# Kernel tuning notes

Measured on AMD Instinct MI355X. Metric: run time of the kernel, lower is better.

## Reference

```python
import jax, jax.numpy as jnp
import numpy as np

HEADS = 16
HEAD_DIM = 64
DIM = 1024
WH, WW = 32, 32
ROPE_DIM = 32  # = HEAD_DIM // 2
ROPE_BASE = 10000
EPS = 1e-6


def _rope_cache():
    # theta: [ROPE_DIM//2]
    theta = 1.0 / (ROPE_BASE ** (jnp.arange(0, ROPE_DIM, 2, dtype=jnp.float32)[: ROPE_DIM // 2] / ROPE_DIM))
    n = WH * WW
    idx = jnp.arange(n, dtype=jnp.float32)
    x_pos = idx % WW
    y_pos = idx // WW
    freqs = jnp.concatenate([x_pos[:, None] * theta[None, :], y_pos[:, None] * theta[None, :]], axis=-1)  # [n, ROPE_DIM]
    return jnp.cos(freqs), jnp.sin(freqs)


def _apply_rope(x, cos, sin):
    # x: [b, h, n, HEAD_DIM] -> pairs [b, h, n, ROPE_DIM, 2]
    xf = x.astype(jnp.float32).reshape(*x.shape[:-1], -1, 2)
    x0, x1 = xf[..., 0], xf[..., 1]
    c = cos[None, None, :, :]
    s = sin[None, None, :, :]
    out = jnp.stack([x0 * c - x1 * s, x1 * c + x0 * s], axis=-1)
    return out.reshape(*x.shape).astype(x.dtype)


def setup_inputs() -> dict:
    key = jax.random.key(0)
    ks = jax.random.split(key, 5)
    b, n = 16, WH * WW
    inner = HEADS * HEAD_DIM
    return {
        "x": jax.random.normal(ks[0], (b, n, DIM), dtype=jnp.float32),
        "t": jax.random.normal(ks[1], (b, DIM), dtype=jnp.float32),
        "norm_w": jnp.ones((DIM,), dtype=jnp.float32),
        "mod_w": jax.random.normal(ks[2], (2 * DIM, DIM), dtype=jnp.float32) * (DIM ** -0.5),
        "qkv_w": jax.random.normal(ks[3], (3 * inner, DIM), dtype=jnp.float32) * (DIM ** -0.5),
        "wo_w": jax.random.normal(ks[4], (DIM, inner), dtype=jnp.float32) * (inner ** -0.5),
    }


def reference(x, t, norm_w, mod_w, qkv_w, wo_w):
    b, n, dim = x.shape
    scale = HEAD_DIM ** -0.5

    # Modulated RMSNorm
    xf = x.astype(jnp.float32)
    xn = (xf * jax.lax.rsqrt(jnp.mean(xf * xf, axis=-1, keepdims=True) + EPS)).astype(x.dtype) * norm_w
    mod = t @ mod_w.T  # [b, 2*dim]
    sc, sh = mod[:, :dim], mod[:, dim:]
    h = xn * (1.0 + sc[:, None, :]) + sh[:, None, :]

    # QKV projection; rearrange 'b n (h d) -> b h n d' with d = 3*HEAD_DIM, THEN chunk
    qkv = h @ qkv_w.T  # [b, n, 3*inner]
    qkv = qkv.reshape(b, n, HEADS, 3 * HEAD_DIM).transpose(0, 2, 1, 3)  # [b, H, n, 3*hd]
    q, k, v = qkv[..., :HEAD_DIM], qkv[..., HEAD_DIM:2 * HEAD_DIM], qkv[..., 2 * HEAD_DIM:]

    # 2D axial RoPE on q, k
    cos, sin = _rope_cache()
    q = _apply_rope(q, cos, sin)
    k = _apply_rope(k, cos, sin)

    # SDPA (non-causal)
    attn = jax.nn.softmax(jnp.einsum('bhqd,bhkd->bhqk', q * scale, k), axis=-1)
    out = jnp.einsum('bhqk,bhkd->bhqd', attn, v)  # [b, H, n, hd]
    out = out.transpose(0, 2, 1, 3).reshape(b, n, HEADS * HEAD_DIM)
    return out @ wo_w.T
```

## Files before the change

kernel.cpp:

```cpp
#include <hip/hip_runtime.h>
#include <stdint.h>

typedef __bf16    bf16x8 __attribute__((ext_vector_type(8)));
typedef float     f32x4  __attribute__((ext_vector_type(4)));
typedef _Float16  f16;
typedef _Float16  f16x2  __attribute__((ext_vector_type(2)));
typedef _Float16  f16x4  __attribute__((ext_vector_type(4)));
typedef _Float16  f16x8  __attribute__((ext_vector_type(8)));

#define DEV __device__ __forceinline__

DEV ushort f2bf(float f) {
  union { float f; uint32_t u; } v; v.f = f;
  uint32_t u = v.u;
  return (ushort)((u + 0x7fffu + ((u >> 16) & 1u)) >> 16);
}

DEV f16x2 cvt_pkrtz(float a, float b) {
  return __builtin_bit_cast(f16x2, __builtin_amdgcn_cvt_pkrtz(a, b));
}

DEV void async16(const void* g, void* l) {
  __builtin_amdgcn_global_load_lds(
      (__attribute__((address_space(1))) void*)(uintptr_t)g,
      (__attribute__((address_space(3))) void*)(uint32_t)(uintptr_t)l,
      16, 0, 0);
}

__global__ __launch_bounds__(256)
void prep_kernel(const float* __restrict__ t, const float* __restrict__ mw,
                 float* __restrict__ mod,
                 const float* __restrict__ qkvw, ushort* __restrict__ wqk,
                 ushort* __restrict__ wv,
                 const float* __restrict__ wow, ushort* __restrict__ wowb) {
  const int id = blockIdx.x;
  const int tid = threadIdx.x;
  if (id < 2048) {
    const int j = id;
    const int w = tid >> 6, lane = tid & 63;
    float wr[16];
#pragma unroll
    for (int i = 0; i < 16; ++i) wr[i] = mw[(size_t)j * 1024 + lane + i * 64];
#pragma unroll
    for (int bb = 0; bb < 4; ++bb) {
      int b = w * 4 + bb;
      float s = 0.f;
#pragma unroll
      for (int i = 0; i < 16; ++i) s += wr[i] * t[b * 1024 + lane + i * 64];
#pragma unroll
      for (int m = 32; m >= 1; m >>= 1) s += __shfl_xor(s, m, 64);
      if (lane == 0) mod[b * 2048 + j] = s;
    }
  } else if (id < 5120) {
    const int j = id - 2048;
    uint32_t hd = (uint32_t)j / 192u;
    uint32_t rem = (uint32_t)j - hd * 192u;
    ushort* dst = (rem < 128u) ? (wqk + (size_t)(hd * 128u + rem) * 1024)
                               : (wv + (size_t)(hd * 64u + (rem - 128u)) * 1024);
    float4 v = ((const float4*)(qkvw + (size_t)j * 1024))[tid];
    ushort4 o;
    o.x = f2bf(v.x); o.y = f2bf(v.y); o.z = f2bf(v.z); o.w = f2bf(v.w);
    ((ushort4*)dst)[tid] = o;
  } else {
    const int i = (id - 5120) * 256 + tid;
    float4 v = ((const float4*)wow)[i];
    ushort4 o;
    o.x = f2bf(v.x); o.y = f2bf(v.y); o.z = f2bf(v.z); o.w = f2bf(v.w);
    ((ushort4*)wowb)[i] = o;
  }
}

__global__ __launch_bounds__(256)
void rms_mod_kernel(const float* __restrict__ x, const float* __restrict__ nw,
                    const float* __restrict__ mod, ushort* __restrict__ h) {
  int row = blockIdx.x;
  int b = row >> 10;
  int tid = threadIdx.x;
  const float4 xv = *(const float4*)(x + (size_t)row * 1024 + tid * 4);
  float ss = xv.x * xv.x + xv.y * xv.y + xv.z * xv.z + xv.w * xv.w;
#pragma unroll
  for (int m = 32; m >= 1; m >>= 1) ss += __shfl_xor(ss, m, 64);
  __shared__ float red[4];
  int w = tid >> 6, lane = tid & 63;
  if (lane == 0) red[w] = ss;
  __syncthreads();
  float tot = red[0] + red[1] + red[2] + red[3];
  float rn = rsqrtf(tot * (1.f / 1024.f) + 1e-6f);
  float4 wv = *(const float4*)(nw + tid * 4);
  float4 sc = *(const float4*)(mod + (size_t)b * 2048 + tid * 4);
  float4 sh = *(const float4*)(mod + (size_t)b * 2048 + 1024 + tid * 4);
  ushort4 o;
  o.x = f2bf(xv.x * rn * wv.x * (1.f + sc.x) + sh.x);
  o.y = f2bf(xv.y * rn * wv.y * (1.f + sc.y) + sh.y);
  o.z = f2bf(xv.z * rn * wv.z * (1.f + sc.z) + sh.z);
  o.w = f2bf(xv.w * rn * wv.w * (1.f + sc.w) + sh.w);
  *(ushort4*)(h + (size_t)row * 1024 + tid * 4) = o;
}

__global__ __launch_bounds__(512, 2)
void gemm_qkv_kernel(const ushort* __restrict__ hbuf, const ushort* __restrict__ wqk,
                     const ushort* __restrict__ wvw,
                     f16* __restrict__ qb, f16* __restrict__ kb,
                     f16* __restrict__ vtb) {
  __shared__ ushort smem[65536];
  const int id0 = blockIdx.x;
  const int id = (id0 & 7) * 96 + (id0 >> 3);
  int mode, m0, n0;
  const ushort *A, *B;
  if (id < 512) {
    mode = 1; m0 = (id >> 3) * 256; n0 = (id & 7) * 256; A = hbuf; B = wqk;
  } else {
    const int i2 = id - 512;
    mode = 2; n0 = (i2 >> 2) * 256; m0 = (i2 & 3) * 256; A = wvw; B = hbuf;
  }
  const int tid = threadIdx.x;
  const int w = tid >> 6, lane = tid & 63, quad = lane >> 4, l15 = lane & 15;
  const int wm = w >> 2, wn = w & 3;

  const int srow = tid >> 3;
  const int sch  = (tid & 7) ^ (srow & 7);
  const int soff = srow * 1024 + sch * 8;
  const ushort* const Abase = A + (size_t)m0 * 1024;
  const ushort* const Bbase = B + (size_t)n0 * 1024;
  ushort* const As0 = smem;
  ushort* const Bs0 = smem + 32768;
  const int sdst = tid * 8;

#define STG_A(d, t, h) do { \
    async16(Abase + (h) * 131072 + soff + (t) * 64,          As0 + (d) * 16384 + (h) * 8192 + sdst); \
    async16(Abase + (h) * 131072 + 65536 + soff + (t) * 64,  As0 + (d) * 16384 + (h) * 8192 + 4096 + sdst); } while (0)
#define STG_B(d, t, h) do { \
    async16(Bbase + (h) * 131072 + soff + (t) * 64,          Bs0 + (d) * 16384 + (h) * 8192 + sdst); \
    async16(Bbase + (h) * 131072 + 65536 + soff + (t) * 64,  Bs0 + (d) * 16384 + (h) * 8192 + 4096 + sdst); } while (0)

  int aoff[2], boff[2];
#pragma unroll
  for (int kk = 0; kk < 2; ++kk) {
    const int swz = (((kk * 4 + quad) ^ (l15 & 7)) * 8);
    aoff[kk] = (wm * 128 + l15) * 64 + swz;
    boff[kk] = (wn * 64 + l15) * 64 + swz;
  }

  const f32x4 fzero = {0.f, 0.f, 0.f, 0.f};
  f32x4 acc[8][4];
#pragma unroll
  for (int a = 0; a < 8; ++a)
#pragma unroll
    for (int b = 0; b < 4; ++b) acc[a][b] = fzero;

  STG_A(0, 0, 0); STG_A(0, 0, 1); STG_B(0, 0, 0); STG_B(0, 0, 1);
  asm volatile("s_waitcnt vmcnt(0)" ::: "memory");
  __builtin_amdgcn_s_barrier();

  bf16x8 af[4][2];
  bf16x8 bfv[2][2];
#pragma unroll 2
  for (int t = 0; t < 16; ++t) {
    const int cur = t & 1, nxt = cur ^ 1;
    const int tn = (t < 15) ? t + 1 : 15;
    const ushort* Asc = As0 + cur * 16384;
    const ushort* Bsc = Bs0 + cur * 16384;

#pragma unroll
    for (int mf = 0; mf < 4; ++mf)
#pragma unroll
      for (int kk = 0; kk < 2; ++kk)
        af[mf][kk] = *(const bf16x8*)(Asc + mf * 1024 + aoff[kk]);
#pragma unroll
    for (int nf = 0; nf < 2; ++nf)
#pragma unroll
      for (int kk = 0; kk < 2; ++kk)
        bfv[nf][kk] = *(const bf16x8*)(Bsc + nf * 1024 + boff[kk]);
    STG_A(nxt, tn, 0);
    __builtin_amdgcn_s_barrier();
    __builtin_amdgcn_s_setprio(1);
#pragma unroll
    for (int mf = 0; mf < 4; ++mf)
#pragma unroll
      for (int nf = 0; nf < 2; ++nf)
#pragma unroll
        for (int kk = 0; kk < 2; ++kk)
          acc[mf][nf] = __builtin_amdgcn_mfma_f32_16x16x32_bf16(
              af[mf][kk], bfv[nf][kk], acc[mf][nf], 0, 0, 0);
    __builtin_amdgcn_s_setprio(0);
    __builtin_amdgcn_s_barrier();

#pragma unroll
    for (int mf = 0; mf < 4; ++mf)
#pragma unroll
      for (int kk = 0; kk < 2; ++kk)
        af[mf][kk] = *(const bf16x8*)(Asc + (4 + mf) * 1024 + aoff[kk]);
    STG_A(nxt, tn, 1);
    __builtin_amdgcn_s_barrier();
    __builtin_amdgcn_s_setprio(1);
#pragma unroll
    for (int mf = 0; mf < 4; ++mf)
#pragma unroll
      for (int nf = 0; nf < 2; ++nf)
#pragma unroll
        for (int kk = 0; kk < 2; ++kk)
          acc[4 + mf][nf] = __builtin_amdgcn_mfma_f32_16x16x32_bf16(
              af[mf][kk], bfv[nf][kk], acc[4 + mf][nf], 0, 0, 0);
    __builtin_amdgcn_s_setprio(0);
    __builtin_amdgcn_s_barrier();

#pragma unroll
    for (int nf = 0; nf < 2; ++nf)
#pragma unroll
      for (int kk = 0; kk < 2; ++kk)
        bfv[nf][kk] = *(const bf16x8*)(Bsc + (2 + nf) * 1024 + boff[kk]);
    STG_B(nxt, tn, 0);
    __builtin_amdgcn_s_barrier();
    __builtin_amdgcn_s_setprio(1);
#pragma unroll
    for (int mf = 0; mf < 4; ++mf)
#pragma unroll
      for (int nf = 0; nf < 2; ++nf)
#pragma unroll
        for (int kk = 0; kk < 2; ++kk)
          acc[4 + mf][2 + nf] = __builtin_amdgcn_mfma_f32_16x16x32_bf16(
              af[mf][kk], bfv[nf][kk], acc[4 + mf][2 + nf], 0, 0, 0);
    __builtin_amdgcn_s_setprio(0);
    __builtin_amdgcn_s_barrier();

#pragma unroll
    for (int mf = 0; mf < 4; ++mf)
#pragma unroll
      for (int kk = 0; kk < 2; ++kk)
        af[mf][kk] = *(const bf16x8*)(Asc + mf * 1024 + aoff[kk]);
    STG_B(nxt, tn, 1);
    __builtin_amdgcn_s_barrier();
    __builtin_amdgcn_s_setprio(1);
#pragma unroll
    for (int mf = 0; mf < 4; ++mf)
#pragma unroll
      for (int nf = 0; nf < 2; ++nf)
#pragma unroll
        for (int kk = 0; kk < 2; ++kk)
          acc[mf][2 + nf] = __builtin_amdgcn_mfma_f32_16x16x32_bf16(
              af[mf][kk], bfv[nf][kk], acc[mf][2 + nf], 0, 0, 0);
    __builtin_amdgcn_s_setprio(0);
    asm volatile("s_waitcnt vmcnt(0)" ::: "memory");
    __builtin_amdgcn_s_barrier();
  }
#undef STG_A
#undef STG_B

  ushort* eps = smem + w * 8192;
#pragma unroll
  for (int mf = 0; mf < 8; ++mf)
#pragma unroll
    for (int nf = 0; nf < 4; ++nf)
#pragma unroll
      for (int r = 0; r < 4; ++r) {
        const int row_loc = mf * 16 + quad * 4 + r;
        const int col = nf * 16 + l15;
        const int ch = (col >> 3) ^ (row_loc & 7);
        union { f16 h; ushort u; } cv;
        cv.h = (f16)acc[mf][nf][r];
        eps[row_loc * 64 + ch * 8 + (col & 7)] = cv.u;
      }

  const int ch = lane & 7;
  const int rbase = lane >> 3;
  const int gcol = n0 + wn * 64;
  if (mode == 1) {
    const int hd = gcol >> 7, part = (gcol >> 6) & 1;
    const float QS = part ? 1.f : 0.125f * 1.44269504f;
    f16* const outp = part ? kb : qb;
    float th[4];
#pragma unroll
    for (int t2 = 0; t2 < 4; ++t2)
      th[t2] = __expf(-(float)((ch * 4 + t2) & 15) * 0.5756462732485114f);
#pragma unroll
    for (int i = 0; i < 16; ++i) {
      const int row_loc = i * 8 + rbase;
      union { uint4 u4; f16 h[8]; } uv;
      uv.u4 = *(const uint4*)(eps + row_loc * 64 + ((ch ^ (row_loc & 7)) * 8));
      const int m = m0 + wm * 128 + row_loc;
      const int n = m & 1023;
      const float xpos = (float)(n & 31), ypos = (float)(n >> 5);
#pragma unroll
      for (int t2 = 0; t2 < 4; ++t2) {
        const int p = ch * 4 + t2;
        const float pos = (p < 16) ? xpos : ypos;
        float sn, cs;
        __sincosf(pos * th[t2], &sn, &cs);
        const float x0 = (float)uv.h[2 * t2], x1 = (float)uv.h[2 * t2 + 1];
        f16x2 ro = cvt_pkrtz((x0 * cs - x1 * sn) * QS, (x1 * cs + x0 * sn) * QS);
        uv.h[2 * t2] = ro[0];
        uv.h[2 * t2 + 1] = ro[1];
      }
      f16* dst = outp + (((size_t)((m >> 10) * 16 + hd) * 1024 + n) * 64 + ch * 8);
      *(uint4*)dst = uv.u4;
    }
  } else {
    const int b = gcol >> 10, tb = gcol & 1023;
#pragma unroll
    for (int i = 0; i < 16; ++i) {
      const int row_loc = i * 8 + rbase;
      const uint4 v = *(const uint4*)(eps + row_loc * 64 + ((ch ^ (row_loc & 7)) * 8));
      const int m = m0 + wm * 128 + row_loc;
      f16* dst = vtb + ((size_t)(b * 1024 + m) * 1024 + tb + ch * 8);
      *(uint4*)dst = v;
    }
  }
}

__global__ __launch_bounds__(256, 3)
void gemm_wo_kernel(const ushort* __restrict__ A, const ushort* __restrict__ B,
                    float* __restrict__ outf) {
  __shared__ ushort smem[8192];
  ushort* As = smem;
  ushort* Bs = smem + 4096;
  const int K = 1024;
  const int m0 = blockIdx.y * 128, n0 = blockIdx.x * 128;
  const int tid = threadIdx.x;
  const int w = tid >> 6, lane = tid & 63, quad = lane >> 4, l15 = lane & 15;
  const int wm = (w >> 1) * 64, wn = (w & 1) * 64;
  const f32x4 fzero = {0.f, 0.f, 0.f, 0.f};
  f32x4 acc[4][4];
#pragma unroll
  for (int a = 0; a < 4; ++a)
#pragma unroll
    for (int b = 0; b < 4; ++b) acc[a][b] = fzero;

  const int s0 = tid, s1 = 256 + tid;
  const int r0 = s0 >> 2, c0 = (s0 & 3) ^ ((r0 >> 1) & 3);
  const int r1 = s1 >> 2, c1 = (s1 & 3) ^ ((r1 >> 1) & 3);
  const int b0 = m0 >> 10, nb = m0 & 1023;
  const size_t Abase = (size_t)b0 * 16 * 1024 * 64;
  const ushort* Ag0 = A + Abase + (size_t)(nb + r0) * 64 + c0 * 8;
  const ushort* Ag1 = A + Abase + (size_t)(nb + r1) * 64 + c1 * 8;
  const ushort* Bg0 = B + (size_t)(n0 + r0) * K + c0 * 8;
  const ushort* Bg1 = B + (size_t)(n0 + r1) * K + c1 * 8;

  for (int kt = 0; kt < K; kt += 32) {
    const size_t ka = (size_t)(kt >> 6) * 65536 + (size_t)(kt & 63);
    async16(Ag0 + ka, As + s0 * 8);
    async16(Ag1 + ka, As + s1 * 8);
    async16(Bg0 + kt, Bs + s0 * 8);
    async16(Bg1 + kt, Bs + s1 * 8);
    __syncthreads();
    bf16x8 af[4], bfr[4];
#pragma unroll
    for (int tm = 0; tm < 4; ++tm) {
      int r = wm + tm * 16 + l15;
      int cs = quad ^ ((r >> 1) & 3);
      af[tm] = *(const bf16x8*)(As + (r * 4 + cs) * 8);
    }
#pragma unroll
    for (int tn = 0; tn < 4; ++tn) {
      int r = wn + tn * 16 + l15;
      int cs = quad ^ ((r >> 1) & 3);
      bfr[tn] = *(const bf16x8*)(Bs + (r * 4 + cs) * 8);
    }
#pragma unroll
    for (int tm = 0; tm < 4; ++tm)
#pragma unroll
      for (int tn = 0; tn < 4; ++tn)
        acc[tm][tn] = __builtin_amdgcn_mfma_f32_16x16x32_bf16(af[tm], bfr[tn],
                                                              acc[tm][tn], 0, 0, 0);
    __syncthreads();
  }

#pragma unroll
  for (int tm = 0; tm < 4; ++tm)
#pragma unroll
    for (int tn = 0; tn < 4; ++tn) {
      int col = n0 + wn + tn * 16 + l15;
#pragma unroll
      for (int r = 0; r < 4; ++r) {
        int row = m0 + wm + tm * 16 + quad * 4 + r;
        outf[(size_t)row * 1024 + col] = acc[tm][tn][r];
      }
    }
}

__global__ __launch_bounds__(256, 3)
void attn_kernel(const f16* __restrict__ qbuf, const f16* __restrict__ kbuf,
                 const f16* __restrict__ vtbuf, ushort* __restrict__ aout) {
  __shared__ f16 Ks[128 * 64];
  __shared__ f16 Vs[64 * 128];

  const int id = blockIdx.x;
  const int xcd = id & 7, j = id >> 3;
  const int bh = xcd * 32 + (j >> 3);
  const int q0 = (j & 7) * 128;
  const f16* Qg = qbuf + (size_t)bh * 1024 * 64;
  const f16* Kg = kbuf + (size_t)bh * 1024 * 64;
  const f16* Vg = vtbuf + (size_t)bh * 64 * 1024;
  const int tid = threadIdx.x;
  const int w = tid >> 6, lane = tid & 63, quad = lane >> 4, l15 = lane & 15;
  const f32x4 fzero = {0.f, 0.f, 0.f, 0.f};

  f16x8 qf[2][2];
#pragma unroll
  for (int qs = 0; qs < 2; ++qs)
#pragma unroll
    for (int dc = 0; dc < 2; ++dc)
      qf[qs][dc] = *(const f16x8*)(Qg + (size_t)(q0 + w * 32 + qs * 16 + l15) * 64 +
                                   dc * 32 + quad * 8);

  f32x4 oacc[2][4];
#pragma unroll
  for (int qs = 0; qs < 2; ++qs)
#pragma unroll
    for (int ds = 0; ds < 4; ++ds) oacc[qs][ds] = fzero;
  float mrun[2] = {-1e30f, -1e30f}, lrun[2] = {0.f, 0.f};

  for (int kt = 0; kt < 1024; kt += 128) {
#pragma unroll
    for (int i = 0; i < 4; ++i) {
      int u = i * 256 + tid, r = u >> 3, c = u & 7;
      async16(Kg + (size_t)(kt + r) * 64 + (c ^ (r & 7)) * 8, Ks + u * 8);
    }
#pragma unroll
    for (int i = 0; i < 4; ++i) {
      int u = i * 256 + tid, r = u >> 4, c = u & 15;
      async16(Vg + (size_t)r * 1024 + kt + (c ^ (r & 15)) * 8, Vs + u * 8);
    }
    __syncthreads();

    f32x4 sacc[2][8];
#pragma unroll
    for (int qs = 0; qs < 2; ++qs)
#pragma unroll
      for (int ks = 0; ks < 8; ++ks) sacc[qs][ks] = fzero;
#pragma unroll
    for (int ks = 0; ks < 8; ++ks) {
#pragma unroll
      for (int dc = 0; dc < 2; ++dc) {
        int row = ks * 16 + l15;
        int ch = (dc * 4 + quad) ^ (row & 7);
        f16x8 kf = *(const f16x8*)(Ks + row * 64 + ch * 8);
        sacc[0][ks] = __builtin_amdgcn_mfma_f32_16x16x32_f16(kf, qf[0][dc], sacc[0][ks], 0, 0, 0);
        sacc[1][ks] = __builtin_amdgcn_mfma_f32_16x16x32_f16(kf, qf[1][dc], sacc[1][ks], 0, 0, 0);
      }
    }

    f16x4 pf[2][8];
#pragma unroll
    for (int qs = 0; qs < 2; ++qs) {
      const float* sv = (const float*)&sacc[qs][0];
      float mx = fmaxf(sv[0], sv[1]);
#pragma unroll
      for (int k = 2; k < 32; k += 2)
        mx = fmaxf(fmaxf(mx, sv[k]), sv[k + 1]);
      mx = fmaxf(mx, __shfl_xor(mx, 16, 64));
      mx = fmaxf(mx, __shfl_xor(mx, 32, 64));
      float mnew = fmaxf(mrun[qs], mx);
      float alpha = exp2f(mrun[qs] - mnew);
      mrun[qs] = mnew;
      float rs = 0.f;
#pragma unroll
      for (int ks = 0; ks < 8; ++ks) {
        float p0 = exp2f(sacc[qs][ks][0] - mnew);
        float p1 = exp2f(sacc[qs][ks][1] - mnew);
        float p2 = exp2f(sacc[qs][ks][2] - mnew);
        float p3 = exp2f(sacc[qs][ks][3] - mnew);
        rs += (p0 + p1) + (p2 + p3);
        union { f16x4 v; f16x2 h[2]; } pu;
        pu.h[0] = cvt_pkrtz(p0, p1);
        pu.h[1] = cvt_pkrtz(p2, p3);
        pf[qs][ks] = pu.v;
      }
      rs += __shfl_xor(rs, 16, 64);
      rs += __shfl_xor(rs, 32, 64);
      lrun[qs] = lrun[qs] * alpha + rs;
      float ar[4];
#pragma unroll
      for (int r = 0; r < 4; ++r) ar[r] = __shfl(alpha, quad * 4 + r, 64);
#pragma unroll
      for (int ds = 0; ds < 4; ++ds)
#pragma unroll
        for (int r = 0; r < 4; ++r) oacc[qs][ds][r] *= ar[r];
    }

#pragma unroll
    for (int ks = 0; ks < 8; ++ks) {
#pragma unroll
      for (int ds = 0; ds < 4; ++ds) {
        int row = ds * 16 + l15;
        int c16 = ks * 2 + (quad >> 1);
        f16x4 vf = *(const f16x4*)(Vs + row * 128 + ((c16 ^ (row & 15)) * 8) + (quad & 1) * 4);
        oacc[0][ds] = __builtin_amdgcn_mfma_f32_16x16x16f16(pf[0][ks], vf, oacc[0][ds], 0, 0, 0);
        oacc[1][ds] = __builtin_amdgcn_mfma_f32_16x16x16f16(pf[1][ks], vf, oacc[1][ds], 0, 0, 0);
      }
    }
    __syncthreads();
  }

  ushort* eps = (ushort*)Ks + w * 2048;
#pragma unroll
  for (int qs = 0; qs < 2; ++qs) {
    float linv[4];
#pragma unroll
    for (int r = 0; r < 4; ++r) linv[r] = 1.f / __shfl(lrun[qs], quad * 4 + r, 64);
#pragma unroll
    for (int ds = 0; ds < 4; ++ds)
#pragma unroll
      for (int r = 0; r < 4; ++r) {
        int row_loc = qs * 16 + quad * 4 + r;
        int col = ds * 16 + l15;
        int ch = (col >> 3) ^ (row_loc & 7);
        eps[row_loc * 64 + ch * 8 + (col & 7)] = f2bf(oacc[qs][ds][r] * linv[r]);
      }
  }
  __syncthreads();
  const size_t obase = ((size_t)bh * 1024 + q0 + w * 32) * 64;
#pragma unroll
  for (int i = 0; i < 4; ++i) {
    int row_loc = i * 8 + (lane >> 3);
    int ch = lane & 7;
    uint4 v = *(const uint4*)(eps + row_loc * 64 + ((ch ^ (row_loc & 7)) * 8));
    *(uint4*)(aout + obase + row_loc * 64 + ch * 8) = v;
  }
}

extern "C" void kernel_launch(void* const* d_in, const int* in_sizes, int n_in,
                              void* d_out, int out_size, void* d_ws, size_t ws_size,
                              hipStream_t stream) {
  const float* x    = (const float*)d_in[0];
  const float* t    = (const float*)d_in[1];
  const float* nw   = (const float*)d_in[2];
  const float* mw   = (const float*)d_in[3];
  const float* qkvw = (const float*)d_in[4];
  const float* wow  = (const float*)d_in[5];
  float* out = (float*)d_out;
  char* ws = (char*)d_ws;

  float*  modbuf  = (float*)(ws);
  ushort* hbuf    = (ushort*)(ws + 131072);
  ushort* wqk_b   = (ushort*)(ws + 33685504);
  ushort* wv_b    = (ushort*)(ws + 37879808);
  ushort* wow_b   = (ushort*)(ws + 39976960);
  f16*    qbuf    = (f16*)(ws + 42074112);
  f16*    kbuf    = (f16*)(ws + 75628544);
  f16*    vtbuf   = (f16*)(ws + 109182976);
  ushort* abuf    = (ushort*)(ws + 142737408);

  prep_kernel<<<dim3(6144), dim3(256), 0, stream>>>(
      t, mw, modbuf, qkvw, wqk_b, wv_b, wow, wow_b);
  rms_mod_kernel<<<dim3(16384), dim3(256), 0, stream>>>(x, nw, modbuf, hbuf);
  gemm_qkv_kernel<<<dim3(768), dim3(512), 0, stream>>>(
      hbuf, wqk_b, wv_b, qbuf, kbuf, vtbuf);
  attn_kernel<<<dim3(2048), dim3(256), 0, stream>>>(qbuf, kbuf, vtbuf, abuf);
  gemm_wo_kernel<<<dim3(8, 128), dim3(256), 0, stream>>>(abuf, wow_b, out);
}
```

Before: 437.4 us.

## Double-buffer attention K/V tiles, lazy softmax rescale, fast exp/rcp, V bank swizzle

The attention kernel now double-buffers K and V tiles in shared memory, prefetching the next tile with async loads while the current one is computed. This doubles LDS use, so the occupancy target drops from 3 to 2 blocks. Softmax now skips the running-max rescale unless the max grows by more than 8, and uses hardware exp2 and rcp intrinsics. The V-transpose store swaps 8-byte halves on odd rows, and the PV loads use a matching half index to reduce LDS bank conflicts. The lazy rescale lets unnormalised values grow up to 2^8, which carries some fp16 overflow risk for P accumulation.

```diff
diff --git a/kernel.cpp b/kernel.cpp
--- a/kernel.cpp
+++ b/kernel.cpp
@@ -299,7 +299,8 @@
 #pragma unroll
     for (int i = 0; i < 16; ++i) {
       const int row_loc = i * 8 + rbase;
-      const uint4 v = *(const uint4*)(eps + row_loc * 64 + ((ch ^ (row_loc & 7)) * 8));
+      uint4 v = *(const uint4*)(eps + row_loc * 64 + ((ch ^ (row_loc & 7)) * 8));
+      if (i & 1) { unsigned t0 = v.x, t1 = v.y; v.x = v.z; v.y = v.w; v.z = t0; v.w = t1; }
       const int m = m0 + wm * 128 + row_loc;
       f16* dst = vtb + ((size_t)(b * 1024 + m) * 1024 + tb + ch * 8);
       *(uint4*)dst = v;
@@ -377,11 +378,11 @@
     }
 }
 
-__global__ __launch_bounds__(256, 3)
+__global__ __launch_bounds__(256, 2)
 void attn_kernel(const f16* __restrict__ qbuf, const f16* __restrict__ kbuf,
                  const f16* __restrict__ vtbuf, ushort* __restrict__ aout) {
-  __shared__ f16 Ks[128 * 64];
-  __shared__ f16 Vs[64 * 128];
+  __shared__ f16 Ks[2][128 * 64];
+  __shared__ f16 Vs[2][64 * 128];
 
   const int id = blockIdx.x;
   const int xcd = id & 7, j = id >> 3;
@@ -409,18 +410,36 @@
     for (int ds = 0; ds < 4; ++ds) oacc[qs][ds] = fzero;
   float mrun[2] = {-1e30f, -1e30f}, lrun[2] = {0.f, 0.f};
 
+#pragma unroll
+  for (int i = 0; i < 4; ++i) {
+    int u = i * 256 + tid, r = u >> 3, c = u & 7;
+    async16(Kg + (size_t)r * 64 + (c ^ (r & 7)) * 8, &Ks[0][u * 8]);
+  }
+#pragma unroll
+  for (int i = 0; i < 4; ++i) {
+    int u = i * 256 + tid, r = u >> 4, c = u & 15;
+    async16(Vg + (size_t)r * 1024 + (c ^ (r & 15)) * 8, &Vs[0][u * 8]);
+  }
+  __syncthreads();
+
+#pragma unroll 2
   for (int kt = 0; kt < 1024; kt += 128) {
-#pragma unroll
-    for (int i = 0; i < 4; ++i) {
-      int u = i * 256 + tid, r = u >> 3, c = u & 7;
-      async16(Kg + (size_t)(kt + r) * 64 + (c ^ (r & 7)) * 8, Ks + u * 8);
-    }
-#pragma unroll
-    for (int i = 0; i < 4; ++i) {
-      int u = i * 256 + tid, r = u >> 4, c = u & 15;
-      async16(Vg + (size_t)r * 1024 + kt + (c ^ (r & 15)) * 8, Vs + u * 8);
-    }
-    __syncthreads();
+    const int cur = (kt >> 7) & 1;
+    if (kt + 128 < 1024) {
+      const int nkt = kt + 128;
+#pragma unroll
+      for (int i = 0; i < 4; ++i) {
+        int u = i * 256 + tid, r = u >> 3, c = u & 7;
+        async16(Kg + (size_t)(nkt + r) * 64 + (c ^ (r & 7)) * 8, &Ks[cur ^ 1][u * 8]);
+      }
+#pragma unroll
+      for (int i = 0; i < 4; ++i) {
+        int u = i * 256 + tid, r = u >> 4, c = u & 15;
+        async16(Vg + (size_t)r * 1024 + nkt + (c ^ (r & 15)) * 8, &Vs[cur ^ 1][u * 8]);
+      }
+    }
+    const f16* Ksc = Ks[cur];
+    const f16* Vsc = Vs[cur];
 
     f32x4 sacc[2][8];
 #pragma unroll
@@ -433,7 +452,7 @@
       for (int dc = 0; dc < 2; ++dc) {
         int row = ks * 16 + l15;
         int ch = (dc * 4 + quad) ^ (row & 7);
-        f16x8 kf = *(const f16x8*)(Ks + row * 64 + ch * 8);
+        f16x8 kf = *(const f16x8*)(Ksc + row * 64 + ch * 8);
         sacc[0][ks] = __builtin_amdgcn_mfma_f32_16x16x32_f16(kf, qf[0][dc], sacc[0][ks], 0, 0, 0);
         sacc[1][ks] = __builtin_amdgcn_mfma_f32_16x16x32_f16(kf, qf[1][dc], sacc[1][ks], 0, 0, 0);
       }
@@ -449,16 +468,27 @@
         mx = fmaxf(fmaxf(mx, sv[k]), sv[k + 1]);
       mx = fmaxf(mx, __shfl_xor(mx, 16, 64));
       mx = fmaxf(mx, __shfl_xor(mx, 32, 64));
-      float mnew = fmaxf(mrun[qs], mx);
-      float alpha = exp2f(mrun[qs] - mnew);
-      mrun[qs] = mnew;
+      if (__any(mx - mrun[qs] > 8.f)) {
+        float mnew = fmaxf(mrun[qs], mx);
+        float alpha = __builtin_amdgcn_exp2f(mrun[qs] - mnew);
+        mrun[qs] = mnew;
+        lrun[qs] *= alpha;
+        float ar[4];
+#pragma unroll
+        for (int r = 0; r < 4; ++r) ar[r] = __shfl(alpha, quad * 4 + r, 64);
+#pragma unroll
+        for (int ds = 0; ds < 4; ++ds)
+#pragma unroll
+          for (int r = 0; r < 4; ++r) oacc[qs][ds][r] *= ar[r];
+      }
+      const float mnew = mrun[qs];
       float rs = 0.f;
 #pragma unroll
       for (int ks = 0; ks < 8; ++ks) {
-        float p0 = exp2f(sacc[qs][ks][0] - mnew);
-        float p1 = exp2f(sacc[qs][ks][1] - mnew);
-        float p2 = exp2f(sacc[qs][ks][2] - mnew);
-        float p3 = exp2f(sacc[qs][ks][3] - mnew);
+        float p0 = __builtin_amdgcn_exp2f(sacc[qs][ks][0] - mnew);
+        float p1 = __builtin_amdgcn_exp2f(sacc[qs][ks][1] - mnew);
+        float p2 = __builtin_amdgcn_exp2f(sacc[qs][ks][2] - mnew);
+        float p3 = __builtin_amdgcn_exp2f(sacc[qs][ks][3] - mnew);
         rs += (p0 + p1) + (p2 + p3);
         union { f16x4 v; f16x2 h[2]; } pu;
         pu.h[0] = cvt_pkrtz(p0, p1);
@@ -467,14 +497,7 @@
       }
       rs += __shfl_xor(rs, 16, 64);
       rs += __shfl_xor(rs, 32, 64);
-      lrun[qs] = lrun[qs] * alpha + rs;
-      float ar[4];
-#pragma unroll
-      for (int r = 0; r < 4; ++r) ar[r] = __shfl(alpha, quad * 4 + r, 64);
-#pragma unroll
-      for (int ds = 0; ds < 4; ++ds)
-#pragma unroll
-        for (int r = 0; r < 4; ++r) oacc[qs][ds][r] *= ar[r];
+      lrun[qs] += rs;
     }
 
 #pragma unroll
@@ -483,7 +506,8 @@
       for (int ds = 0; ds < 4; ++ds) {
         int row = ds * 16 + l15;
         int c16 = ks * 2 + (quad >> 1);
-        f16x4 vf = *(const f16x4*)(Vs + row * 128 + ((c16 ^ (row & 15)) * 8) + (quad & 1) * 4);
+        int half = (quad & 1) ^ ((l15 >> 3) & 1);
+        f16x4 vf = *(const f16x4*)(Vsc + row * 128 + ((c16 ^ (row & 15)) * 8) + half * 4);
         oacc[0][ds] = __builtin_amdgcn_mfma_f32_16x16x16f16(pf[0][ks], vf, oacc[0][ds], 0, 0, 0);
         oacc[1][ds] = __builtin_amdgcn_mfma_f32_16x16x16f16(pf[1][ks], vf, oacc[1][ds], 0, 0, 0);
       }
@@ -491,12 +515,13 @@
     __syncthreads();
   }
 
-  ushort* eps = (ushort*)Ks + w * 2048;
+  ushort* eps = (ushort*)&Ks[0][0] + w * 2048;
 #pragma unroll
   for (int qs = 0; qs < 2; ++qs) {
     float linv[4];
 #pragma unroll
-    for (int r = 0; r < 4; ++r) linv[r] = 1.f / __shfl(lrun[qs], quad * 4 + r, 64);
+    for (int r = 0; r < 4; ++r)
+      linv[r] = __builtin_amdgcn_rcpf(__shfl(lrun[qs], quad * 4 + r, 64));
 #pragma unroll
     for (int ds = 0; ds < 4; ++ds)
 #pragma unroll
```

New measurement: 406.0 us. 1.08x faster.
